# Optimization experiments

Measured on AMD Instinct MI355X. Metric: run time of the kernel, lower is better.

Reference implementation:

```python
import jax, jax.numpy as jnp
import numpy as np

N = 50000          # nodes
E = 800000         # random edges (self-loops added in reference, per PyG default)
B = 64             # graphs in batch
IN_DIM = 773
HID = 256
OUT = 128
H1, D1 = 4, 64     # heads, head_dim layer 1 (256 = 4*64)
H2, D2 = 4, 32     # heads, head_dim layer 2 (128 = 4*32)
NEG_SLOPE = 0.2


def setup_inputs() -> dict:
    key = jax.random.key(0)
    ks = jax.random.split(key, 20)
    s = 0.02
    x = jax.random.normal(ks[0], (N, IN_DIM), dtype=jnp.float32)
    edge_index = jax.random.randint(ks[1], (2, E), 0, N, dtype=jnp.int32)
    batch = jnp.sort(jax.random.randint(ks[2], (N,), 0, B, dtype=jnp.int32))
    return {
        "x": x,
        "edge_index": edge_index,
        "batch": batch,
        "W_in": jax.random.normal(ks[3], (IN_DIM, HID), jnp.float32) * s,
        "b_in": jnp.zeros((HID,), jnp.float32),
        "W1": jax.random.normal(ks[4], (HID, H1 * D1), jnp.float32) * s,
        "att_src1": jax.random.normal(ks[5], (H1, D1), jnp.float32) * s,
        "att_dst1": jax.random.normal(ks[6], (H1, D1), jnp.float32) * s,
        "b1": jnp.zeros((H1 * D1,), jnp.float32),
        "W2": jax.random.normal(ks[7], (HID, H2 * D2), jnp.float32) * s,
        "att_src2": jax.random.normal(ks[8], (H2, D2), jnp.float32) * s,
        "att_dst2": jax.random.normal(ks[9], (H2, D2), jnp.float32) * s,
        "b2": jnp.zeros((H2 * D2,), jnp.float32),
        "W_cls": jax.random.normal(ks[10], (OUT, 2), jnp.float32) * s,
        "b_cls": jnp.zeros((2,), jnp.float32),
        "W_conf": jax.random.normal(ks[11], (OUT, 1), jnp.float32) * s,
        "b_conf": jnp.zeros((1,), jnp.float32),
    }


def _gat_layer(h, src, dst, W, att_src, att_dst, bias, heads, dim):
    # h: (N, F_in). PyG GATConv, concat=True, eval mode (dropout off).
    hW = (h @ W).reshape(N, heads, dim)                    # (N, H, D)
    a_src = jnp.einsum("nhd,hd->nh", hW, att_src)          # (N, H)
    a_dst = jnp.einsum("nhd,hd->nh", hW, att_dst)
    e = a_src[src] + a_dst[dst]                            # (E', H)
    e = jax.nn.leaky_relu(e, NEG_SLOPE)
    # segment softmax over incoming edges of each dst node
    m = jax.ops.segment_max(e, dst, num_segments=N)        # (N, H)
    ex = jnp.exp(e - m[dst])
    z = jax.ops.segment_sum(ex, dst, num_segments=N)       # (N, H)
    alpha = ex / (z[dst] + 1e-16)                          # (E', H)
    msg = hW[src] * alpha[:, :, None]                      # (E', H, D)
    out = jax.ops.segment_sum(msg, dst, num_segments=N)    # (N, H, D)
    return out.reshape(N, heads * dim) + bias


def reference(x, edge_index, batch, W_in, b_in,
              W1, att_src1, att_dst1, b1,
              W2, att_src2, att_dst2, b2,
              W_cls, b_cls, W_conf, b_conf):
    loops = jnp.arange(N, dtype=edge_index.dtype)
    src = jnp.concatenate([edge_index[0], loops])
    dst = jnp.concatenate([edge_index[1], loops])

    h = jax.nn.relu(x @ W_in + b_in)                       # (N, 256)
    h = jax.nn.relu(_gat_layer(h, src, dst, W1, att_src1, att_dst1, b1, H1, D1))
    h = _gat_layer(h, src, dst, W2, att_src2, att_dst2, b2, H2, D2)
    h = jax.nn.relu(h)                                     # (N, 128)

    # global mean pool over graphs
    sums = jax.ops.segment_sum(h, batch, num_segments=B)   # (B, 128)
    cnts = jax.ops.segment_sum(jnp.ones((N,), h.dtype), batch, num_segments=B)
    graph_emb = sums / jnp.maximum(cnts, 1.0)[:, None]

    class_logits = graph_emb @ W_cls + b_cls               # (B, 2)
    confidence = jax.nn.sigmoid(graph_emb @ W_conf + b_conf)  # (B, 1)
    return class_logits, confidence
```

## Files before the change

### kernel.cpp

```cpp
#include <hip/hip_runtime.h>
#include <math.h>

#define NN 50000
#define NE 800000
#define NB 64
#define IND 773
#define MPAD 50048
#define SCAN_B 196

typedef __attribute__((ext_vector_type(8))) short short8_t;
typedef __attribute__((ext_vector_type(4))) float f32x4;
typedef __attribute__((ext_vector_type(2))) float f32x2;

__device__ __forceinline__ float lrelu(float x) { return x > 0.f ? x : 0.2f * x; }
__device__ __forceinline__ short f2b(float f) {
    unsigned u = __float_as_uint(f);
    unsigned r = (u + 0x7fffu + ((u >> 16) & 1u)) >> 16;
    return (short)r;
}
__device__ __forceinline__ float b2f(short s) {
    return __uint_as_float(((unsigned)(unsigned short)s) << 16);
}
__device__ __forceinline__ unsigned char enc8(float v) {
    return (unsigned char)(__builtin_amdgcn_cvt_pk_fp8_f32(v, v, 0, false) & 0xff);
}
__device__ __forceinline__ unsigned pack4fp8(float a, float b, float c, float d) {
    unsigned w = 0;
    w = __builtin_amdgcn_cvt_pk_fp8_f32(a, b, w, false);
    w = __builtin_amdgcn_cvt_pk_fp8_f32(c, d, w, true);
    return w;
}
__device__ __forceinline__ void dec4(unsigned w, float* v) {
    f32x2 lo = __builtin_amdgcn_cvt_pk_f32_fp8((int)w, false);
    f32x2 hi = __builtin_amdgcn_cvt_pk_f32_fp8((int)w, true);
    v[0] = lo[0]; v[1] = lo[1]; v[2] = hi[0]; v[3] = hi[1];
}
__device__ __forceinline__ void dec2(unsigned w, float* v) {
    f32x2 lo = __builtin_amdgcn_cvt_pk_f32_fp8((int)w, false);
    v[0] = lo[0]; v[1] = lo[1];
}

#define GLOAD16(g, l) __builtin_amdgcn_global_load_lds(                         \
    (const __attribute__((address_space(1))) void*)(g),                         \
    (__attribute__((address_space(3))) void*)(l), 16, 0, 0)

__global__ __launch_bounds__(512) void gemm_a(const float* __restrict__ X,
                                              const short* __restrict__ Bt,
                                              const float* __restrict__ bias,
                                              unsigned char* __restrict__ C8) {
    const int K = 800, N = 256, NT = 25;
    __shared__ short As[2][128 * 32];
    __shared__ short Bs[2][256 * 32];
    const int t = threadIdx.x;
    const int w = t >> 6, l = t & 63;
    const int l15 = l & 15, lh = l >> 4;
    const int bm = blockIdx.x * 128;
    const int wr = (w >> 2) * 64, wc = (w & 3) * 64;
    const int arow = t >> 2, acb = (t & 3) * 8;
    const int gm = bm + arow;
    const bool rowok = gm < NN;
    const float* xrow = X + (size_t)gm * IND;
    const short* bG = Bt + (size_t)(t >> 2) * K + (t & 3) * 8;

    f32x4 acc[4][4];
#pragma unroll
    for (int i = 0; i < 4; ++i)
#pragma unroll
        for (int j = 0; j < 4; ++j) acc[i][j] = (f32x4){0.f, 0.f, 0.f, 0.f};

    short8_t rA;
    auto loadA = [&](int it) {
        int gk = it * 32 + acb;
        if (rowok && gk + 7 < IND) {
            float4 v0 = *(const float4*)(xrow + gk);
            float4 v1 = *(const float4*)(xrow + gk + 4);
            rA[0] = f2b(v0.x); rA[1] = f2b(v0.y); rA[2] = f2b(v0.z); rA[3] = f2b(v0.w);
            rA[4] = f2b(v1.x); rA[5] = f2b(v1.y); rA[6] = f2b(v1.z); rA[7] = f2b(v1.w);
        } else {
#pragma unroll
            for (int j = 0; j < 8; ++j)
                rA[j] = (rowok && gk + j < IND) ? f2b(xrow[gk + j]) : (short)0;
        }
    };
    auto stageB = [&](int buf, int it) {
        GLOAD16(bG + it * 32, &Bs[buf][w * 512]);
        GLOAD16(bG + (size_t)128 * K + it * 32, &Bs[buf][128 * 32 + w * 512]);
    };

    loadA(0);
    stageB(0, 0);
    stageB(1, 1);
    *(short8_t*)&As[0][arow * 32 + acb] = rA;
    loadA(1);
    __syncthreads();

    for (int it = 0; it < NT; ++it) {
        const int c = it & 1, n = c ^ 1;
        short8_t af[4], bfr[4];
#pragma unroll
        for (int mi = 0; mi < 4; ++mi)
            af[mi] = *(const short8_t*)&As[c][(wr + mi * 16 + l15) * 32 + lh * 8];
#pragma unroll
        for (int ni = 0; ni < 4; ++ni)
            bfr[ni] = *(const short8_t*)&Bs[c][(wc + ni * 16 + l15) * 32 + lh * 8];
        if (it + 1 < NT) *(short8_t*)&As[n][arow * 32 + acb] = rA;
#pragma unroll
        for (int mi = 0; mi < 4; ++mi)
#pragma unroll
            for (int ni = 0; ni < 4; ++ni)
                acc[mi][ni] = __builtin_amdgcn_mfma_f32_16x16x32_bf16(af[mi], bfr[ni], acc[mi][ni], 0, 0, 0);
        __syncthreads();
        if (it + 2 < NT) {
            loadA(it + 2);
            stageB(c, it + 2);
        }
    }

    char* R = (char*)Bs;
#pragma unroll
    for (int mi = 0; mi < 4; ++mi) {
#pragma unroll
        for (int r = 0; r < 4; ++r) {
            int rloc = wr + mi * 16 + lh * 4 + r;
#pragma unroll
            for (int ni = 0; ni < 4; ++ni) {
                int gcol = wc + ni * 16 + l15;
                float v = fmaxf(acc[mi][ni][r] + bias[gcol], 0.f);
                R[rloc * 256 + gcol] = (char)enc8(v);
            }
        }
    }
    __syncthreads();
#pragma unroll
    for (int i = 0; i < 4; ++i) {
        int idx = i * 512 + t;
        int row = idx >> 4, cb = (idx & 15) * 16;
        int grow = bm + row;
        if (grow < NN)
            *(float4*)&C8[(size_t)grow * N + cb] = *(float4*)&R[row * 256 + cb];
    }
}

__global__ __launch_bounds__(256) void gemm_b(const unsigned char* __restrict__ A8,
                                              const unsigned char* __restrict__ B8,
                                              const float* __restrict__ att_s,
                                              const float* __restrict__ att_d,
                                              unsigned char* __restrict__ C8,
                                              float* __restrict__ a_s,
                                              float* __restrict__ a_d) {
    const int K = 256, N = 256, NT = 8;
    __shared__ char LDS8[16384];
    const int t = threadIdx.x;
    const int w = t >> 6, l = t & 63;
    const int l15 = l & 15, lh = l >> 4;
    const int bm = blockIdx.x * 128, bn = blockIdx.y * 128;
    const int wr = (w >> 1) * 64, wc = (w & 1) * 64;

    const unsigned char* aG = A8 + (size_t)(bm + w * 32 + (l >> 1)) * K + (l & 1) * 16;
    const unsigned char* bG = B8 + (size_t)(bn + w * 32 + (l >> 1)) * K + (l & 1) * 16;

    auto stage = [&](int buf, int k0) {
        GLOAD16(aG + k0, LDS8 + buf * 4096 + w * 1024);
        GLOAD16(bG + k0, LDS8 + 8192 + buf * 4096 + w * 1024);
    };

    f32x4 acc[4][4];
#pragma unroll
    for (int i = 0; i < 4; ++i)
#pragma unroll
        for (int j = 0; j < 4; ++j) acc[i][j] = (f32x4){0.f, 0.f, 0.f, 0.f};

    stage(0, 0);
    stage(1, 32);
    __syncthreads();

    for (int it = 0; it < NT; ++it) {
        const int c = it & 1;
        long af[4], bfr[4];
#pragma unroll
        for (int mi = 0; mi < 4; ++mi)
            af[mi] = *(const long*)&LDS8[c * 4096 + (wr + mi * 16 + l15) * 32 + lh * 8];
#pragma unroll
        for (int ni = 0; ni < 4; ++ni)
            bfr[ni] = *(const long*)&LDS8[8192 + c * 4096 + (wc + ni * 16 + l15) * 32 + lh * 8];
#pragma unroll
        for (int mi = 0; mi < 4; ++mi)
#pragma unroll
            for (int ni = 0; ni < 4; ++ni)
                acc[mi][ni] = __builtin_amdgcn_mfma_f32_16x16x32_fp8_fp8(af[mi], bfr[ni], acc[mi][ni], 0, 0, 0);
        __syncthreads();
        if (it + 2 < NT) stage(c, (it + 2) * 32);
    }

    const int head = (bn + wc) >> 6;
    float sa[4], sd[4];
#pragma unroll
    for (int ni = 0; ni < 4; ++ni) {
        sa[ni] = att_s[head * 64 + ni * 16 + l15];
        sd[ni] = att_d[head * 64 + ni * 16 + l15];
    }
    char* R = LDS8;
#pragma unroll
    for (int mi = 0; mi < 4; ++mi) {
#pragma unroll
        for (int r = 0; r < 4; ++r) {
            int rloc = wr + mi * 16 + lh * 4 + r;
            int grow = bm + rloc;
            float s = acc[mi][0][r] * sa[0] + acc[mi][1][r] * sa[1] +
                      acc[mi][2][r] * sa[2] + acc[mi][3][r] * sa[3];
            float d = acc[mi][0][r] * sd[0] + acc[mi][1][r] * sd[1] +
                      acc[mi][2][r] * sd[2] + acc[mi][3][r] * sd[3];
#pragma unroll
            for (int off = 1; off < 16; off <<= 1) {
                s += __shfl_xor(s, off);
                d += __shfl_xor(d, off);
            }
            if (grow < NN && l15 == 0) { a_s[grow * 4 + head] = s; a_d[grow * 4 + head] = d; }
#pragma unroll
            for (int ni = 0; ni < 4; ++ni)
                R[rloc * 128 + wc + ni * 16 + l15] = (char)enc8(acc[mi][ni][r]);
        }
    }
    __syncthreads();
#pragma unroll
    for (int i = 0; i < 4; ++i) {
        int idx = i * 256 + t;
        int row = idx >> 3, cb = (idx & 7) * 16;
        int grow = bm + row;
        if (grow < NN)
            *(float4*)&C8[(size_t)grow * N + bn + cb] = *(float4*)&R[row * 128 + cb];
    }
}

__global__ __launch_bounds__(256) void gemm_c(const unsigned char* __restrict__ A8,
                                              const unsigned char* __restrict__ B8,
                                              const float* __restrict__ att_s,
                                              const float* __restrict__ att_d,
                                              unsigned char* __restrict__ C8,
                                              float* __restrict__ a_s,
                                              float* __restrict__ a_d) {
    const int K = 256, N = 128, NT = 8;
    __shared__ char LDS8[16384];
    const int t = threadIdx.x;
    const int w = t >> 6, l = t & 63;
    const int l15 = l & 15, lh = l >> 4;
    const int bm = blockIdx.x * 128;
    const int wr = (w >> 1) * 64, wc = (w & 1) * 64;

    const unsigned char* aG = A8 + (size_t)(bm + w * 32 + (l >> 1)) * K + (l & 1) * 16;
    const unsigned char* bG = B8 + (size_t)(w * 32 + (l >> 1)) * K + (l & 1) * 16;

    auto stage = [&](int buf, int k0) {
        GLOAD16(aG + k0, LDS8 + buf * 4096 + w * 1024);
        GLOAD16(bG + k0, LDS8 + 8192 + buf * 4096 + w * 1024);
    };

    f32x4 acc[4][4];
#pragma unroll
    for (int i = 0; i < 4; ++i)
#pragma unroll
        for (int j = 0; j < 4; ++j) acc[i][j] = (f32x4){0.f, 0.f, 0.f, 0.f};

    stage(0, 0);
    stage(1, 32);
    __syncthreads();

    for (int it = 0; it < NT; ++it) {
        const int c = it & 1;
        long af[4], bfr[4];
#pragma unroll
        for (int mi = 0; mi < 4; ++mi)
            af[mi] = *(const long*)&LDS8[c * 4096 + (wr + mi * 16 + l15) * 32 + lh * 8];
#pragma unroll
        for (int ni = 0; ni < 4; ++ni)
            bfr[ni] = *(const long*)&LDS8[8192 + c * 4096 + (wc + ni * 16 + l15) * 32 + lh * 8];
#pragma unroll
        for (int mi = 0; mi < 4; ++mi)
#pragma unroll
            for (int ni = 0; ni < 4; ++ni)
                acc[mi][ni] = __builtin_amdgcn_mfma_f32_16x16x32_fp8_fp8(af[mi], bfr[ni], acc[mi][ni], 0, 0, 0);
        __syncthreads();
        if (it + 2 < NT) stage(c, (it + 2) * 32);
    }

    const int h0 = wc >> 5;
    float sa[4], sd[4];
#pragma unroll
    for (int ni = 0; ni < 4; ++ni) {
        int idx = (h0 + (ni >> 1)) * 32 + (ni & 1) * 16 + l15;
        sa[ni] = att_s[idx];
        sd[ni] = att_d[idx];
    }
    char* R = LDS8;
#pragma unroll
    for (int mi = 0; mi < 4; ++mi) {
#pragma unroll
        for (int r = 0; r < 4; ++r) {
            int rloc = wr + mi * 16 + lh * 4 + r;
            int grow = bm + rloc;
            float s0 = acc[mi][0][r] * sa[0] + acc[mi][1][r] * sa[1];
            float s1 = acc[mi][2][r] * sa[2] + acc[mi][3][r] * sa[3];
            float d0 = acc[mi][0][r] * sd[0] + acc[mi][1][r] * sd[1];
            float d1 = acc[mi][2][r] * sd[2] + acc[mi][3][r] * sd[3];
#pragma unroll
            for (int off = 1; off < 16; off <<= 1) {
                s0 += __shfl_xor(s0, off); s1 += __shfl_xor(s1, off);
                d0 += __shfl_xor(d0, off); d1 += __shfl_xor(d1, off);
            }
            if (grow < NN && l15 == 0) {
                a_s[grow * 4 + h0] = s0; a_s[grow * 4 + h0 + 1] = s1;
                a_d[grow * 4 + h0] = d0; a_d[grow * 4 + h0 + 1] = d1;
            }
#pragma unroll
            for (int ni = 0; ni < 4; ++ni)
                R[rloc * 128 + wc + ni * 16 + l15] = (char)enc8(acc[mi][ni][r]);
        }
    }
    __syncthreads();
#pragma unroll
    for (int i = 0; i < 4; ++i) {
        int idx = i * 256 + t;
        int row = idx >> 3, cb = (idx & 7) * 16;
        int grow = bm + row;
        if (grow < NN)
            *(float4*)&C8[(size_t)grow * N + cb] = *(float4*)&R[row * 128 + cb];
    }
}

__global__ __launch_bounds__(256) void k_prep(const float* __restrict__ W_in,
                                              const float* __restrict__ W1,
                                              const float* __restrict__ W2,
                                              short* __restrict__ Wt_in,
                                              unsigned char* __restrict__ Wt1,
                                              unsigned char* __restrict__ Wt2,
                                              int* __restrict__ deg,
                                              float* __restrict__ emb) {
    int b = blockIdx.x;
    const float* W; int K, N, Kp, kb, nb, fp8;
    short* Wts = nullptr; unsigned char* Wt8 = nullptr;
    if (b < 200)      { W = W_in; Wts = Wt_in; fp8 = 0; K = IND; N = 256; Kp = 800; kb = (b % 25) * 32; nb = (b / 25) * 32; }
    else if (b < 264) { b -= 200; W = W1; Wt8 = Wt1; fp8 = 1; K = 256; N = 256; Kp = 256; kb = (b % 8) * 32; nb = (b / 8) * 32; }
    else if (b < 296) { b -= 264; W = W2; Wt8 = Wt2; fp8 = 1; K = 256; N = 128; Kp = 256; kb = (b % 8) * 32; nb = (b / 8) * 32; }
    else {
        int i = (b - 296) * 256 + threadIdx.x;
        if (i < NN) deg[i] = 0;
        if (i < NB * 128) emb[i] = 0.f;
        return;
    }
    __shared__ float tile[32][33];
    int tx = threadIdx.x & 31, ty = threadIdx.x >> 5;
#pragma unroll
    for (int r = 0; r < 32; r += 8) {
        int k = kb + ty + r;
        tile[ty + r][tx] = (k < K) ? W[(size_t)k * N + nb + tx] : 0.f;
    }
    __syncthreads();
#pragma unroll
    for (int r = 0; r < 32; r += 8) {
        int n = nb + ty + r, k = kb + tx;
        float v = tile[tx][ty + r];
        if (fp8) Wt8[(size_t)n * Kp + k] = enc8(v);
        else     Wts[(size_t)n * Kp + k] = f2b(v);
    }
}

__global__ void k_hist(const int* __restrict__ ei, int* __restrict__ deg) {
    int e = blockIdx.x * 256 + threadIdx.x;
    if (e >= NE) return;
    atomicAdd(&deg[ei[NE + e]], 1);
}

__global__ __launch_bounds__(256) void k_bsum(const int* __restrict__ deg,
                                              int* __restrict__ bsum) {
    int i = blockIdx.x * 256 + threadIdx.x;
    int v = (i < NN) ? deg[i] : 0;
#pragma unroll
    for (int off = 32; off; off >>= 1) v += __shfl_down(v, off);
    __shared__ int ws[4];
    if ((threadIdx.x & 63) == 0) ws[threadIdx.x >> 6] = v;
    __syncthreads();
    if (threadIdx.x == 0) bsum[blockIdx.x] = ws[0] + ws[1] + ws[2] + ws[3];
}

__global__ __launch_bounds__(256) void k_scan3(const int* __restrict__ deg,
                                               const int* __restrict__ bsum,
                                               int* __restrict__ rowp,
                                               int* __restrict__ cursor) {
    int b = blockIdx.x;
    int i = b * 256 + threadIdx.x;
    int d = (i < NN) ? deg[i] : 0;
    __shared__ int sb[SCAN_B];
    if (threadIdx.x < SCAN_B) sb[threadIdx.x] = bsum[threadIdx.x];
    int v = d;
    int lane = threadIdx.x & 63, wid = threadIdx.x >> 6;
#pragma unroll
    for (int off = 1; off < 64; off <<= 1) {
        int u = __shfl_up(v, off);
        if (lane >= off) v += u;
    }
    __shared__ int ws[4];
    if (lane == 63) ws[wid] = v;
    __syncthreads();
    int add = 0;
    for (int q = 0; q < b; ++q) add += sb[q];
    for (int wq = 0; wq < wid; ++wq) add += ws[wq];
    int excl = add + v - d;
    if (i < NN) { rowp[i] = excl; cursor[i] = excl; }
    if (i == NN - 1) rowp[NN] = excl + d;
}

__global__ void k_scatter(const int* __restrict__ ei, int* __restrict__ cursor,
                          int* __restrict__ colidx) {
    int e = blockIdx.x * 256 + threadIdx.x;
    if (e >= NE) return;
    int s = ei[e], d = ei[NE + e];
    int pos = atomicAdd(&cursor[d], 1);
    colidx[pos] = s;
}

template<int HD, int OUT8>
__global__ __launch_bounds__(256) void gat_agg(const unsigned char* __restrict__ hW8,
                                               const float* __restrict__ a_s,
                                               const float* __restrict__ a_d,
                                               const int* __restrict__ row_ptr,
                                               const int* __restrict__ colidx,
                                               const float* __restrict__ bias,
                                               void* __restrict__ outp) {
    const int CPL = HD / 64;
    int node = blockIdx.x * 4 + (threadIdx.x >> 6);
    int lane = threadIdx.x & 63;
    if (node >= NN) return;
    int h = lane >> 4;
    int start = row_ptr[node], end = row_ptr[node + 1];
    float adst = a_d[node * 4 + h];
    float eself = lrelu(a_s[node * 4 + h] + adst);

    float z = 1.f;
    float acc[CPL];
    {
        const unsigned char* row = hW8 + (size_t)node * HD + lane * CPL;
        if (CPL == 4) dec4(*(const unsigned*)row, acc);
        else          dec2(*(const unsigned short*)row, acc);
    }
    for (int e = start; e < end; e += 8) {
        int sidx[8];
        float xs[8], ex[8];
#pragma unroll
        for (int q = 0; q < 8; ++q) {
            int ee = e + q;
            sidx[q] = colidx[ee < end ? ee : end - 1];
        }
#pragma unroll
        for (int q = 0; q < 8; ++q) xs[q] = a_s[sidx[q] * 4 + h];
        float v[8][CPL];
        if (CPL == 4) {
#pragma unroll
            for (int q = 0; q < 8; ++q)
                dec4(*(const unsigned*)(hW8 + (size_t)sidx[q] * HD + lane * 4), v[q]);
        } else {
#pragma unroll
            for (int q = 0; q < 8; ++q)
                dec2(*(const unsigned short*)(hW8 + (size_t)sidx[q] * HD + lane * 2), v[q]);
        }
#pragma unroll
        for (int q = 0; q < 8; ++q) {
            float wq = __expf(lrelu(xs[q] + adst) - eself);
            ex[q] = (e + q < end) ? wq : 0.f;
        }
#pragma unroll
        for (int q = 0; q < 8; ++q) z += ex[q];
#pragma unroll
        for (int j = 0; j < CPL; ++j) {
            float a = 0.f;
#pragma unroll
            for (int q = 0; q < 8; ++q) a += ex[q] * v[q][j];
            acc[j] += a;
        }
    }
    float inv = 1.f / z;
    float o[CPL];
#pragma unroll
    for (int j = 0; j < CPL; ++j)
        o[j] = fmaxf(acc[j] * inv + bias[lane * CPL + j], 0.f);
    if (OUT8) {
        unsigned* orow = (unsigned*)((unsigned char*)outp + (size_t)node * HD + lane * 4);
        *orow = pack4fp8(o[0], o[1], (CPL == 4 ? o[2] : 0.f), (CPL == 4 ? o[3] : 0.f));
    } else {
        short* orow = (short*)outp + (size_t)node * HD + lane * CPL;
#pragma unroll
        for (int j = 0; j < CPL; ++j) orow[j] = f2b(o[j]);
    }
}

__global__ __launch_bounds__(128) void k_pool(const short* __restrict__ h2,
                                              const int* __restrict__ batch,
                                              float* __restrict__ emb) {
    int b = blockIdx.x >> 2;
    int chunk = blockIdx.x & 3;
    int t = threadIdx.x;
    int lo = 0, hi = NN;
    while (lo < hi) { int mid = (lo + hi) >> 1; if (batch[mid] < b) lo = mid + 1; else hi = mid; }
    int start = lo;
    lo = 0; hi = NN;
    while (lo < hi) { int mid = (lo + hi) >> 1; if (batch[mid] < b + 1) lo = mid + 1; else hi = mid; }
    int end = lo;
    float s = 0.f;
    for (int n = start + chunk; n < end; n += 4) s += b2f(h2[(size_t)n * 128 + t]);
    atomicAdd(&emb[b * 128 + t], s);
}

__global__ __launch_bounds__(128) void k_head(const float* __restrict__ emb,
                                              const int* __restrict__ batch,
                                              const float* __restrict__ W_cls,
                                              const float* __restrict__ b_cls,
                                              const float* __restrict__ W_conf,
                                              const float* __restrict__ b_conf,
                                              float* __restrict__ out) {
    int b = blockIdx.x;
    int t = threadIdx.x;
    int lo = 0, hi = NN;
    while (lo < hi) { int mid = (lo + hi) >> 1; if (batch[mid] < b) lo = mid + 1; else hi = mid; }
    int start = lo;
    lo = 0; hi = NN;
    while (lo < hi) { int mid = (lo + hi) >> 1; if (batch[mid] < b + 1) lo = mid + 1; else hi = mid; }
    int end = lo;
    __shared__ float se[128];
    se[t] = emb[b * 128 + t] / fmaxf((float)(end - start), 1.f);
    __syncthreads();
    if (t == 0) {
        float v = b_cls[0];
        for (int c = 0; c < 128; ++c) v += se[c] * W_cls[c * 2 + 0];
        out[b * 2 + 0] = v;
    } else if (t == 1) {
        float v = b_cls[1];
        for (int c = 0; c < 128; ++c) v += se[c] * W_cls[c * 2 + 1];
        out[b * 2 + 1] = v;
    } else if (t == 2) {
        float v = b_conf[0];
        for (int c = 0; c < 128; ++c) v += se[c] * W_conf[c];
        out[128 + b] = 1.f / (1.f + expf(-v));
    }
}

extern "C" void kernel_launch(void* const* d_in, const int* in_sizes, int n_in,
                              void* d_out, int out_size, void* d_ws, size_t ws_size,
                              hipStream_t stream) {
    const float* x        = (const float*)d_in[0];
    const int*   ei       = (const int*)d_in[1];
    const int*   batch    = (const int*)d_in[2];
    const float* W_in     = (const float*)d_in[3];
    const float* b_in     = (const float*)d_in[4];
    const float* W1       = (const float*)d_in[5];
    const float* att_src1 = (const float*)d_in[6];
    const float* att_dst1 = (const float*)d_in[7];
    const float* b1       = (const float*)d_in[8];
    const float* W2       = (const float*)d_in[9];
    const float* att_src2 = (const float*)d_in[10];
    const float* att_dst2 = (const float*)d_in[11];
    const float* b2       = (const float*)d_in[12];
    const float* W_cls    = (const float*)d_in[13];
    const float* b_cls    = (const float*)d_in[14];
    const float* W_conf   = (const float*)d_in[15];
    const float* b_conf   = (const float*)d_in[16];
    float* out = (float*)d_out;

    char* ws = (char*)d_ws;
    unsigned char* h0  = (unsigned char*)(ws + 0);
    unsigned char* hW1 = (unsigned char*)(ws + 12812288);
    unsigned char* h1  = (unsigned char*)(ws + 25624576);
    unsigned char* hW2 = (unsigned char*)(ws + 38436864);
    short*         h2  = (short*)(ws + 44843008);
    size_t base = 57655296;
    short*         Wt_in = (short*)(ws + base);
    unsigned char* Wt1   = (unsigned char*)(ws + base + 409600);
    unsigned char* Wt2   = (unsigned char*)(ws + base + 475136);
    float* a_s1  = (float*)(ws + base + 507904);
    float* a_d1  = (float*)(ws + base + 1307904);
    float* emb   = (float*)(ws + base + 2107904);
    int*   deg    = (int*)(ws + base + 2140672);
    int*   rowp   = (int*)(ws + base + 2340672);
    int*   cursor = (int*)(ws + base + 2540736);
    int*   colidx = (int*)(ws + base + 2740736);
    int*   bsum   = (int*)(ws + base + 5940736);

    k_prep<<<296 + SCAN_B, 256, 0, stream>>>(W_in, W1, W2, Wt_in, Wt1, Wt2, deg, emb);
    k_hist<<<NE / 256, 256, 0, stream>>>(ei, deg);
    k_bsum<<<SCAN_B, 256, 0, stream>>>(deg, bsum);
    k_scan3<<<SCAN_B, 256, 0, stream>>>(deg, bsum, rowp, cursor);
    k_scatter<<<NE / 256, 256, 0, stream>>>(ei, cursor, colidx);

    gemm_a<<<391, 512, 0, stream>>>(x, Wt_in, b_in, h0);
    gemm_b<<<dim3(391, 2), 256, 0, stream>>>(h0, Wt1, att_src1, att_dst1, hW1, a_s1, a_d1);
    gat_agg<256, 1><<<12500, 256, 0, stream>>>(hW1, a_s1, a_d1, rowp, colidx, b1, h1);
    gemm_c<<<391, 256, 0, stream>>>(h1, Wt2, att_src2, att_dst2, hW2, a_s1, a_d1);
    gat_agg<128, 0><<<12500, 256, 0, stream>>>(hW2, a_s1, a_d1, rowp, colidx, b2, h2);
    k_pool<<<NB * 4, 128, 0, stream>>>(h2, batch, emb);
    k_head<<<NB, 128, 0, stream>>>(emb, batch, W_cls, b_cls, W_conf, b_conf, out);
}
```

Baseline: 343.5 us.

## Restructure input GEMM to feed A fragments from registers with 1024-thread blocks

The first dense projection kernel now uses 16 waves per block. Each wave owns a 16-row strip and a 128-column half, and loads its A operand straight from global fp32 into MFMA registers instead of staging it through LDS. This removes the A shared-memory buffer and its write/read traffic and doubles the waves available to hide latency. In exchange, each A row is loaded twice (once per column half), per-wave MFMA work drops to 8 per k-step with lower B fragment reuse, and the 1024-thread blocks may limit occupancy.

```diff
diff --git a/kernel.cpp b/kernel.cpp
--- a/kernel.cpp
+++ b/kernel.cpp
@@ -44,96 +44,84 @@
     (const __attribute__((address_space(1))) void*)(g),                         \
     (__attribute__((address_space(3))) void*)(l), 16, 0, 0)
 
-__global__ __launch_bounds__(512) void gemm_a(const float* __restrict__ X,
-                                              const short* __restrict__ Bt,
-                                              const float* __restrict__ bias,
-                                              unsigned char* __restrict__ C8) {
+__global__ __launch_bounds__(1024) void gemm_a(const float* __restrict__ X,
+                                               const short* __restrict__ Bt,
+                                               const float* __restrict__ bias,
+                                               unsigned char* __restrict__ C8) {
     const int K = 800, N = 256, NT = 25;
-    __shared__ short As[2][128 * 32];
     __shared__ short Bs[2][256 * 32];
     const int t = threadIdx.x;
     const int w = t >> 6, l = t & 63;
     const int l15 = l & 15, lh = l >> 4;
     const int bm = blockIdx.x * 128;
-    const int wr = (w >> 2) * 64, wc = (w & 3) * 64;
-    const int arow = t >> 2, acb = (t & 3) * 8;
-    const int gm = bm + arow;
-    const bool rowok = gm < NN;
-    const float* xrow = X + (size_t)gm * IND;
+    const int strip = (w & 7) * 16;
+    const int ch = (w >> 3) * 128;
+    const int arow = bm + strip + l15;
+    const bool rowok = arow < NN;
+    const float* xrow = X + (size_t)arow * IND;
     const short* bG = Bt + (size_t)(t >> 2) * K + (t & 3) * 8;
 
-    f32x4 acc[4][4];
-#pragma unroll
-    for (int i = 0; i < 4; ++i)
-#pragma unroll
-        for (int j = 0; j < 4; ++j) acc[i][j] = (f32x4){0.f, 0.f, 0.f, 0.f};
-
-    short8_t rA;
-    auto loadA = [&](int it) {
-        int gk = it * 32 + acb;
+    f32x4 acc[8];
+#pragma unroll
+    for (int i = 0; i < 8; ++i) acc[i] = (f32x4){0.f, 0.f, 0.f, 0.f};
+
+    short8_t rA0, rA1;
+    auto loadA = [&](int it, short8_t& r) {
+        int gk = it * 32 + lh * 8;
         if (rowok && gk + 7 < IND) {
             float4 v0 = *(const float4*)(xrow + gk);
             float4 v1 = *(const float4*)(xrow + gk + 4);
-            rA[0] = f2b(v0.x); rA[1] = f2b(v0.y); rA[2] = f2b(v0.z); rA[3] = f2b(v0.w);
-            rA[4] = f2b(v1.x); rA[5] = f2b(v1.y); rA[6] = f2b(v1.z); rA[7] = f2b(v1.w);
+            r[0] = f2b(v0.x); r[1] = f2b(v0.y); r[2] = f2b(v0.z); r[3] = f2b(v0.w);
+            r[4] = f2b(v1.x); r[5] = f2b(v1.y); r[6] = f2b(v1.z); r[7] = f2b(v1.w);
         } else {
 #pragma unroll
             for (int j = 0; j < 8; ++j)
-                rA[j] = (rowok && gk + j < IND) ? f2b(xrow[gk + j]) : (short)0;
+                r[j] = (rowok && gk + j < IND) ? f2b(xrow[gk + j]) : (short)0;
         }
     };
     auto stageB = [&](int buf, int it) {
         GLOAD16(bG + it * 32, &Bs[buf][w * 512]);
-        GLOAD16(bG + (size_t)128 * K + it * 32, &Bs[buf][128 * 32 + w * 512]);
     };
 
-    loadA(0);
+#define GAITER(IT, CC, RCUR)                                                            \
+    {                                                                                   \
+        _Pragma("unroll")                                                               \
+        for (int ni = 0; ni < 8; ++ni) {                                                \
+            short8_t bf = *(const short8_t*)&Bs[CC][(ch + ni * 16 + l15) * 32 + lh * 8];\
+            acc[ni] = __builtin_amdgcn_mfma_f32_16x16x32_bf16(RCUR, bf, acc[ni], 0, 0, 0); \
+        }                                                                               \
+        __syncthreads();                                                                \
+        if ((IT) + 2 < NT) { loadA((IT) + 2, RCUR); stageB(CC, (IT) + 2); }             \
+    }
+
+    loadA(0, rA0);
     stageB(0, 0);
     stageB(1, 1);
-    *(short8_t*)&As[0][arow * 32 + acb] = rA;
-    loadA(1);
-    __syncthreads();
-
-    for (int it = 0; it < NT; ++it) {
-        const int c = it & 1, n = c ^ 1;
-        short8_t af[4], bfr[4];
-#pragma unroll
-        for (int mi = 0; mi < 4; ++mi)
-            af[mi] = *(const short8_t*)&As[c][(wr + mi * 16 + l15) * 32 + lh * 8];
-#pragma unroll
-        for (int ni = 0; ni < 4; ++ni)
-            bfr[ni] = *(const short8_t*)&Bs[c][(wc + ni * 16 + l15) * 32 + lh * 8];
-        if (it + 1 < NT) *(short8_t*)&As[n][arow * 32 + acb] = rA;
-#pragma unroll
-        for (int mi = 0; mi < 4; ++mi)
-#pragma unroll
-            for (int ni = 0; ni < 4; ++ni)
-                acc[mi][ni] = __builtin_amdgcn_mfma_f32_16x16x32_bf16(af[mi], bfr[ni], acc[mi][ni], 0, 0, 0);
-        __syncthreads();
-        if (it + 2 < NT) {
-            loadA(it + 2);
-            stageB(c, it + 2);
-        }
-    }
+    loadA(1, rA1);
+    __syncthreads();
+
+    for (int it = 0; it < NT - 1; it += 2) {
+        GAITER(it, 0, rA0);
+        GAITER(it + 1, 1, rA1);
+    }
+    GAITER(NT - 1, 0, rA0);
+#undef GAITER
 
     char* R = (char*)Bs;
 #pragma unroll
-    for (int mi = 0; mi < 4; ++mi) {
+    for (int ni = 0; ni < 8; ++ni) {
 #pragma unroll
         for (int r = 0; r < 4; ++r) {
-            int rloc = wr + mi * 16 + lh * 4 + r;
-#pragma unroll
-            for (int ni = 0; ni < 4; ++ni) {
-                int gcol = wc + ni * 16 + l15;
-                float v = fmaxf(acc[mi][ni][r] + bias[gcol], 0.f);
-                R[rloc * 256 + gcol] = (char)enc8(v);
-            }
-        }
-    }
-    __syncthreads();
-#pragma unroll
-    for (int i = 0; i < 4; ++i) {
-        int idx = i * 512 + t;
+            int rloc = strip + lh * 4 + r;
+            int gcol = ch + ni * 16 + l15;
+            float v = fmaxf(acc[ni][r] + bias[gcol], 0.f);
+            R[rloc * 256 + gcol] = (char)enc8(v);
+        }
+    }
+    __syncthreads();
+#pragma unroll
+    for (int i = 0; i < 2; ++i) {
+        int idx = i * 1024 + t;
         int row = idx >> 4, cb = (idx & 15) * 16;
         int grow = bm + row;
         if (grow < NN)
@@ -589,7 +577,7 @@
     k_scan3<<<SCAN_B, 256, 0, stream>>>(deg, bsum, rowp, cursor);
     k_scatter<<<NE / 256, 256, 0, stream>>>(ei, cursor, colidx);
 
-    gemm_a<<<391, 512, 0, stream>>>(x, Wt_in, b_in, h0);
+    gemm_a<<<391, 1024, 0, stream>>>(x, Wt_in, b_in, h0);
     gemm_b<<<dim3(391, 2), 256, 0, stream>>>(h0, Wt1, att_src1, att_dst1, hW1, a_s1, a_d1);
     gat_agg<256, 1><<<12500, 256, 0, stream>>>(hW1, a_s1, a_d1, rowp, colidx, b1, h1);
     gemm_c<<<391, 256, 0, stream>>>(h1, Wt2, att_src2, att_dst2, hW2, a_s1, a_d1);
```

After: 367.4 us. 1.07x slower.
